# Performance work log

Hardware: AMD Instinct MI355X
Metric: run time of the kernel (lower is better)

Reference implementation:

```python
import jax, jax.numpy as jnp
import numpy as np

EPS = 1e-5
TEMPERATURE = 0.07

def _layernorm(x, g, b):
    m = jnp.mean(x, axis=-1, keepdims=True)
    v = jnp.mean(jnp.square(x - m), axis=-1, keepdims=True)
    return (x - m) * jax.lax.rsqrt(v + EPS) * g + b

def _proj(x, W, b, g, beta):
    # Linear -> LayerNorm -> ReLU (Dropout is identity in eval)
    return jax.nn.relu(_layernorm(x @ W + b, g, beta))

def setup_inputs() -> dict:
    key = jax.random.key(0)
    B, S, Dv, Dl, D = 8, 2048, 768, 768, 768
    ks = jax.random.split(key, 8)
    def lin(k, din, dout):
        return jax.random.normal(k, (din, dout), jnp.float32) / np.sqrt(din)
    return {
        "vision_features": jax.random.normal(ks[0], (B, S, Dv), jnp.float32),
        "language_features": jax.random.normal(ks[1], (B, S, Dl), jnp.float32),
        "vW": lin(ks[2], Dv, D), "vb": jnp.zeros((D,), jnp.float32),
        "vg": jnp.ones((D,), jnp.float32), "vbeta": jnp.zeros((D,), jnp.float32),
        "lW": lin(ks[3], Dl, D), "lb": jnp.zeros((D,), jnp.float32),
        "lg": jnp.ones((D,), jnp.float32), "lbeta": jnp.zeros((D,), jnp.float32),
        "claw": lin(ks[4], D, D),  # claw_matrix parameter [D, D]
        "oW": lin(ks[5], 2 * D, D), "ob": jnp.zeros((D,), jnp.float32),
        "og": jnp.ones((D,), jnp.float32), "obeta": jnp.zeros((D,), jnp.float32),
    }

def reference(vision_features, language_features, vW, vb, vg, vbeta,
              lW, lb, lg, lbeta, claw, oW, ob, og, obeta):
    vp = _proj(vision_features, vW, vb, vg, vbeta)      # [B,S,D]
    lp = _proj(language_features, lW, lb, lg, lbeta)    # [B,S,D]
    # similarity / temperature, scaled by mean of learned claw matrix
    sim = jnp.einsum('bsd,btd->bst', vp, lp) * (claw.mean() / TEMPERATURE)
    A = jax.nn.softmax(sim, axis=-1)                    # [B,S,S] claw matrix
    aligned_vision = jnp.einsum('bst,btd->bsd', A, vp)  # A @ vp
    aligned_language = jnp.einsum('bst,bsd->btd', A, lp)  # A^T @ lp
    combined = jnp.concatenate([aligned_vision, aligned_language], axis=-1)
    return jax.nn.relu(_layernorm(combined @ oW + ob, og, obeta))
```

## Files before the change

### kernel.cpp

```cpp
#include <hip/hip_runtime.h>
#include <hip/hip_bf16.h>

typedef short short8 __attribute__((ext_vector_type(8)));
typedef float f32x4 __attribute__((ext_vector_type(4)));
typedef unsigned short u16;

#define BK 32
static __device__ __forceinline__ int sw(int row, int g) {
  return row * 32 + ((g ^ ((row >> 3) & 3)) << 3);
}

static __device__ __forceinline__ u16 f2b(float f) {
  union { float f; unsigned u; } x; x.f = f;
  unsigned r = x.u + 0x7FFF + ((x.u >> 16) & 1);
  return (u16)(r >> 16);
}
static __device__ __forceinline__ float b2f(u16 u) {
  unsigned int x = ((unsigned int)u) << 16;
  float f; __builtin_memcpy(&f, &x, 4);
  return f;
}

static __device__ __forceinline__ void load8(const u16* p, u16* dst) {
  union { uint4 u; u16 h[8]; } t;
  t.u = *(const uint4*)p;
  #pragma unroll
  for (int j = 0; j < 8; ++j) dst[j] = t.h[j];
}
static __device__ __forceinline__ void load8(const float* p, u16* dst) {
  float4 a = ((const float4*)p)[0];
  float4 b = ((const float4*)p)[1];
  dst[0] = f2b(a.x); dst[1] = f2b(a.y); dst[2] = f2b(a.z); dst[3] = f2b(a.w);
  dst[4] = f2b(b.x); dst[5] = f2b(b.y); dst[6] = f2b(b.z); dst[7] = f2b(b.w);
}

static __device__ __forceinline__ void gl_lds16(const u16* g, u16* l) {
  __builtin_amdgcn_global_load_lds(
      (const __attribute__((address_space(1))) unsigned int*)g,
      (__attribute__((address_space(3))) unsigned int*)l, 16, 0, 0);
}

template<int MA, int MB, typename TyA, typename TyB, typename OutT>
__global__ __launch_bounds__(256) void gemm128(
    const TyA* __restrict__ A, const TyB* __restrict__ B,
    const float* __restrict__ bias, const float* __restrict__ alpha_ptr,
    OutT* __restrict__ C, int K, int lda, int ldb, int ldc,
    long long sA, long long sB, long long sC)
{
  __shared__ u16 As[128 * 32];
  __shared__ u16 Bs[128 * 32];

  A += (long long)blockIdx.z * sA;
  B += (long long)blockIdx.z * sB;
  C += (long long)blockIdx.z * sC;

  const int tid  = threadIdx.x;
  const int m0   = blockIdx.y * 128;
  const int n0   = blockIdx.x * 128;
  const int w    = tid >> 6, lane = tid & 63;
  const int wm   = (w >> 1) * 64;
  const int wn   = (w & 1) * 64;
  const int lrow = lane & 15;
  const int lg   = lane >> 4;

  int aoff[4], boff[4];
  #pragma unroll
  for (int t = 0; t < 4; ++t) {
    const int ar = wm + t * 16 + lrow;
    const int br = wn + t * 16 + lrow;
    aoff[t] = (MA == 1) ? sw(ar, lg) : ar * 32 + lg * 8;
    boff[t] = (MB == 1) ? sw(br, lg) : br * 32 + lg * 8;
  }

  f32x4 acc[4][4] = {};

  for (int k0 = 0; k0 < K; k0 += BK) {
    if constexpr (MA == 0) {
      gl_lds16(A + (long long)(m0 + (tid >> 2)) * lda + (k0 + (tid & 3) * 8),
               As + tid * 8);
      gl_lds16(A + (long long)(m0 + 64 + (tid >> 2)) * lda + (k0 + (tid & 3) * 8),
               As + 2048 + tid * 8);
    } else if constexpr (MA == 1) {
      const int kk = tid >> 3;
      #pragma unroll
      for (int p = 0; p < 2; ++p) {
        const int rr = (tid & 7) * 8 + p * 64;
        u16 h[8];
        load8(A + (long long)(k0 + kk) * lda + (m0 + rr), h);
        #pragma unroll
        for (int j = 0; j < 8; ++j) As[sw(rr + j, kk >> 3) + (kk & 7)] = h[j];
      }
    } else {
      const int g = tid & 3;
      #pragma unroll
      for (int p = 0; p < 2; ++p) {
        const int r = (tid >> 2) + p * 64;
        union { uint4 u; u16 h[8]; } t;
        load8(A + (long long)(m0 + r) * lda + (k0 + g * 8), t.h);
        *(uint4*)(As + r * 32 + g * 8) = t.u;
      }
    }
    if constexpr (MB == 0) {
      gl_lds16(B + (long long)(n0 + (tid >> 2)) * ldb + (k0 + (tid & 3) * 8),
               Bs + tid * 8);
      gl_lds16(B + (long long)(n0 + 64 + (tid >> 2)) * ldb + (k0 + (tid & 3) * 8),
               Bs + 2048 + tid * 8);
    } else {
      const int kk = tid >> 3;
      #pragma unroll
      for (int p = 0; p < 2; ++p) {
        const int rr = (tid & 7) * 8 + p * 64;
        u16 h[8];
        load8(B + (long long)(k0 + kk) * ldb + (n0 + rr), h);
        #pragma unroll
        for (int j = 0; j < 8; ++j) Bs[sw(rr + j, kk >> 3) + (kk & 7)] = h[j];
      }
    }
    __syncthreads();

    short8 af[4], bf[4];
    #pragma unroll
    for (int t = 0; t < 4; ++t) af[t] = *(const short8*)(As + aoff[t]);
    #pragma unroll
    for (int t = 0; t < 4; ++t) bf[t] = *(const short8*)(Bs + boff[t]);
    #pragma unroll
    for (int mt = 0; mt < 4; ++mt)
      #pragma unroll
      for (int nt = 0; nt < 4; ++nt)
        acc[mt][nt] = __builtin_amdgcn_mfma_f32_16x16x32_bf16(
            af[mt], bf[nt], acc[mt][nt], 0, 0, 0);
    __syncthreads();
  }

  const float alpha = alpha_ptr ? *alpha_ptr : 1.0f;
  #pragma unroll
  for (int nt = 0; nt < 4; ++nt) {
    const int n = n0 + wn + nt * 16 + lrow;
    const float bv = bias ? bias[n] : 0.0f;
    #pragma unroll
    for (int mt = 0; mt < 4; ++mt) {
      #pragma unroll
      for (int r = 0; r < 4; ++r) {
        const int m = m0 + wm + mt * 16 + lg * 4 + r;
        C[(long long)m * ldc + n] = OutT(acc[mt][nt][r] * alpha + bv);
      }
    }
  }
}

template<typename OutT>
__global__ __launch_bounds__(256) void ln_relu_kernel(
    const float* __restrict__ x, const float* __restrict__ g,
    const float* __restrict__ beta, OutT* __restrict__ out)
{
  __shared__ float sa[4], sb[4];
  const float* xr = x + (long long)blockIdx.x * 768;
  float v[3]; float s = 0.f, ss = 0.f;
  #pragma unroll
  for (int j = 0; j < 3; ++j) {
    v[j] = xr[threadIdx.x + j * 256];
    s += v[j]; ss += v[j] * v[j];
  }
  #pragma unroll
  for (int off = 32; off; off >>= 1) {
    s  += __shfl_down(s, off);
    ss += __shfl_down(ss, off);
  }
  const int w = threadIdx.x >> 6, lane = threadIdx.x & 63;
  if (!lane) { sa[w] = s; sb[w] = ss; }
  __syncthreads();
  s  = sa[0] + sa[1] + sa[2] + sa[3];
  ss = sb[0] + sb[1] + sb[2] + sb[3];
  const float mean = s * (1.f / 768.f);
  const float var  = ss * (1.f / 768.f) - mean * mean;
  const float rst  = rsqrtf(var + 1e-5f);
  OutT* orow = out + (long long)blockIdx.x * 768;
  #pragma unroll
  for (int j = 0; j < 3; ++j) {
    const int idx = threadIdx.x + j * 256;
    const float yv = (v[j] - mean) * rst * g[idx] + beta[idx];
    const float rv = (yv <= 0.f) ? 0.f : yv;
    orow[idx] = OutT(rv);
  }
}

__global__ __launch_bounds__(256) void softmax_kernel(u16* __restrict__ sim)
{
  __shared__ float sm[4], ssum[4];
  u16* row = sim + (long long)blockIdx.x * 2048;
  union { uint4 u; u16 h[8]; } v;
  v.u = *(const uint4*)(row + threadIdx.x * 8);
  float f[8]; float mx = -1e30f;
  #pragma unroll
  for (int j = 0; j < 8; ++j) { f[j] = b2f(v.h[j]); mx = fmaxf(mx, f[j]); }
  #pragma unroll
  for (int off = 32; off; off >>= 1) mx = fmaxf(mx, __shfl_down(mx, off));
  const int w = threadIdx.x >> 6, lane = threadIdx.x & 63;
  if (!lane) sm[w] = mx;
  __syncthreads();
  mx = fmaxf(fmaxf(sm[0], sm[1]), fmaxf(sm[2], sm[3]));
  float s = 0.f;
  #pragma unroll
  for (int j = 0; j < 8; ++j) { f[j] = __expf(f[j] - mx); s += f[j]; }
  #pragma unroll
  for (int off = 32; off; off >>= 1) s += __shfl_down(s, off);
  if (!lane) ssum[w] = s;
  __syncthreads();
  s = ssum[0] + ssum[1] + ssum[2] + ssum[3];
  const float inv = 1.f / s;
  #pragma unroll
  for (int j = 0; j < 8; ++j) v.h[j] = f2b(f[j] * inv);
  *(uint4*)(row + threadIdx.x * 8) = v.u;
}

__global__ __launch_bounds__(256) void claw_partial_kernel(
    const float* __restrict__ claw, float* __restrict__ partial, int n)
{
  __shared__ float sa[4];
  float s = 0.f;
  const int nv = n >> 2;
  for (int i = blockIdx.x * 256 + threadIdx.x; i < nv; i += 64 * 256) {
    float4 v = ((const float4*)claw)[i];
    s += v.x + v.y + v.z + v.w;
  }
  #pragma unroll
  for (int off = 32; off; off >>= 1) s += __shfl_down(s, off);
  const int w = threadIdx.x >> 6, lane = threadIdx.x & 63;
  if (!lane) sa[w] = s;
  __syncthreads();
  if (threadIdx.x == 0)
    partial[blockIdx.x] = sa[0] + sa[1] + sa[2] + sa[3];
}

__global__ void claw_final_kernel(
    const float* __restrict__ partial, float* __restrict__ scale, float inv)
{
  float s = partial[threadIdx.x];
  #pragma unroll
  for (int off = 32; off; off >>= 1) s += __shfl_down(s, off);
  if (threadIdx.x == 0) *scale = s * inv;
}

extern "C" void kernel_launch(void* const* d_in, const int* in_sizes, int n_in,
                              void* d_out, int out_size, void* d_ws, size_t ws_size,
                              hipStream_t stream)
{
  const float* vis   = (const float*)d_in[0];
  const float* lang  = (const float*)d_in[1];
  const float* vW    = (const float*)d_in[2];
  const float* vb    = (const float*)d_in[3];
  const float* vg    = (const float*)d_in[4];
  const float* vbeta = (const float*)d_in[5];
  const float* lW    = (const float*)d_in[6];
  const float* lb    = (const float*)d_in[7];
  const float* lg    = (const float*)d_in[8];
  const float* lbeta = (const float*)d_in[9];
  const float* claw  = (const float*)d_in[10];
  const float* oW    = (const float*)d_in[11];
  const float* ob    = (const float*)d_in[12];
  const float* og    = (const float*)d_in[13];
  const float* obeta = (const float*)d_in[14];
  float* out = (float*)d_out;

  constexpr int NB = 8, S = 2048, D = 768;
  constexpr int R = NB * S;
  constexpr long long SD = (long long)S * D;
  constexpr long long SS = (long long)S * S;
  const int nclaw = in_sizes[10];
  const float claw_inv = 1.0f / ((float)nclaw * 0.07f);
  const dim3 blk(256);

  char* ws = (char*)d_ws;
  u16*   vp      = (u16*)  (ws);
  u16*   lp      = (u16*)  (ws + 25165824);
  u16*   comb    = (u16*)  (ws + 50331648);
  u16*   sim     = (u16*)  (ws + 100663296);
  float* y       = (float*)(ws + 100663296);
  float* scale   = (float*)(ws + 167772160);
  float* partial = (float*)(ws + 167772176);

  claw_partial_kernel<<<64, blk, 0, stream>>>(claw, partial, nclaw);
  claw_final_kernel<<<1, 64, 0, stream>>>(partial, scale, claw_inv);

  gemm128<2, 1, float, float, float>
      <<<dim3(D / 128, R / 128, 1), blk, 0, stream>>>(
      vis, vW, vb, nullptr, y, D, D, D, D, 0, 0, 0);
  ln_relu_kernel<__hip_bfloat16><<<R, blk, 0, stream>>>(
      y, vg, vbeta, (__hip_bfloat16*)vp);

  gemm128<2, 1, float, float, float>
      <<<dim3(D / 128, R / 128, 1), blk, 0, stream>>>(
      lang, lW, lb, nullptr, y, D, D, D, D, 0, 0, 0);
  ln_relu_kernel<__hip_bfloat16><<<R, blk, 0, stream>>>(
      y, lg, lbeta, (__hip_bfloat16*)lp);

  gemm128<0, 0, u16, u16, __hip_bfloat16>
      <<<dim3(S / 128, S / 128, NB), blk, 0, stream>>>(
      vp, lp, nullptr, scale, (__hip_bfloat16*)sim, D, D, D, S, SD, SD, SS);
  softmax_kernel<<<R, blk, 0, stream>>>(sim);

  gemm128<0, 1, u16, u16, __hip_bfloat16>
      <<<dim3(D / 128, S / 128, NB), blk, 0, stream>>>(
      sim, vp, nullptr, nullptr, (__hip_bfloat16*)comb,
      S, S, D, 2 * D, SS, SD, 2 * SD);
  gemm128<1, 1, u16, u16, __hip_bfloat16>
      <<<dim3(D / 128, S / 128, NB), blk, 0, stream>>>(
      sim, lp, nullptr, nullptr, (__hip_bfloat16*)comb + D,
      S, S, D, 2 * D, SS, SD, 2 * SD);

  gemm128<0, 1, u16, float, float>
      <<<dim3(D / 128, R / 128, 1), blk, 0, stream>>>(
      comb, oW, ob, nullptr, y, 2 * D, 2 * D, D, D, 0, 0, 0);
  ln_relu_kernel<float><<<R, blk, 0, stream>>>(y, og, obeta, out);
}
```

Before: 675.8 us.

## Pre-transpose B operands and pre-convert fp32 inputs to bf16 for async LDS loads

Adds transpose and fp32-to-bf16 conversion kernels so that every GEMM can use the direct global-to-LDS load path (MA=0/MB=0) for B, and for A in all but the A^T GEMM. Before this, the GEMMs used scalar strided loads with per-element LDS scatter. Weights, inputs, vp and lp are transposed or converted ahead of time. The workspace is reused aggressively, with comb aliasing vp and vpT aliasing visb. The cost is the extra transpose and convert passes over global memory.

```diff
diff --git a/kernel.cpp b/kernel.cpp
--- a/kernel.cpp
+++ b/kernel.cpp
@@ -40,9 +40,9 @@
       (__attribute__((address_space(3))) unsigned int*)l, 16, 0, 0);
 }
 
-template<int MA, int MB, typename TyA, typename TyB, typename OutT>
+template<int MA, int MB, typename OutT>
 __global__ __launch_bounds__(256) void gemm128(
-    const TyA* __restrict__ A, const TyB* __restrict__ B,
+    const u16* __restrict__ A, const u16* __restrict__ B,
     const float* __restrict__ bias, const float* __restrict__ alpha_ptr,
     OutT* __restrict__ C, int K, int lda, int ldb, int ldc,
     long long sA, long long sB, long long sC)
@@ -80,7 +80,7 @@
                As + tid * 8);
       gl_lds16(A + (long long)(m0 + 64 + (tid >> 2)) * lda + (k0 + (tid & 3) * 8),
                As + 2048 + tid * 8);
-    } else if constexpr (MA == 1) {
+    } else {
       const int kk = tid >> 3;
       #pragma unroll
       for (int p = 0; p < 2; ++p) {
@@ -89,15 +89,6 @@
         load8(A + (long long)(k0 + kk) * lda + (m0 + rr), h);
         #pragma unroll
         for (int j = 0; j < 8; ++j) As[sw(rr + j, kk >> 3) + (kk & 7)] = h[j];
-      }
-    } else {
-      const int g = tid & 3;
-      #pragma unroll
-      for (int p = 0; p < 2; ++p) {
-        const int r = (tid >> 2) + p * 64;
-        union { uint4 u; u16 h[8]; } t;
-        load8(A + (long long)(m0 + r) * lda + (k0 + g * 8), t.h);
-        *(uint4*)(As + r * 32 + g * 8) = t.u;
       }
     }
     if constexpr (MB == 0) {
@@ -148,6 +139,49 @@
   }
 }
 
+template<typename T>
+__global__ __launch_bounds__(256) void transpose_kernel(
+    const T* __restrict__ in, u16* __restrict__ out, int R, int C,
+    long long sIn, long long sOut)
+{
+  __shared__ u16 t[64][66];
+  in  += (long long)blockIdx.z * sIn;
+  out += (long long)blockIdx.z * sOut;
+  const int r0 = blockIdx.y * 64, c0 = blockIdx.x * 64;
+  const int tid = threadIdx.x;
+  const int rr = tid >> 3, cc = (tid & 7) * 8;
+  #pragma unroll
+  for (int p = 0; p < 2; ++p) {
+    union { uint4 u; unsigned w[4]; u16 h[8]; } v;
+    const int row = rr + p * 32;
+    load8(in + (long long)(r0 + row) * C + (c0 + cc), v.h);
+    #pragma unroll
+    for (int k = 0; k < 4; ++k)
+      *(unsigned*)&t[row][cc + k * 2] = v.w[k];
+  }
+  __syncthreads();
+  #pragma unroll
+  for (int p = 0; p < 2; ++p) {
+    const int oc = (tid >> 3) + p * 32;
+    const int rc = (tid & 7) * 8;
+    union { uint4 u; u16 h[8]; } g;
+    #pragma unroll
+    for (int j = 0; j < 8; ++j) g.h[j] = t[rc + j][oc];
+    *(uint4*)(out + (long long)(c0 + oc) * R + (r0 + rc)) = g.u;
+  }
+}
+
+__global__ __launch_bounds__(256) void cvt_kernel(
+    const float* __restrict__ in, u16* __restrict__ out, int n8)
+{
+  const int stride = gridDim.x * 256;
+  for (int i = blockIdx.x * 256 + threadIdx.x; i < n8; i += stride) {
+    union { uint4 u; u16 h[8]; } v;
+    load8(in + (long long)i * 8, v.h);
+    *(uint4*)(out + (long long)i * 8) = v.u;
+  }
+}
+
 template<typename OutT>
 __global__ __launch_bounds__(256) void ln_relu_kernel(
     const float* __restrict__ x, const float* __restrict__ g,
@@ -271,45 +305,60 @@
   const dim3 blk(256);
 
   char* ws = (char*)d_ws;
-  u16*   vp      = (u16*)  (ws);
-  u16*   lp      = (u16*)  (ws + 25165824);
-  u16*   comb    = (u16*)  (ws + 50331648);
-  u16*   sim     = (u16*)  (ws + 100663296);
-  float* y       = (float*)(ws + 100663296);
+  u16*   vp    = (u16*)  (ws);
+  u16*   lp    = (u16*)  (ws + 25165824);
+  u16*   visb  = (u16*)  (ws + 50331648);
+  u16*   vpT   = (u16*)  (ws + 50331648);
+  u16*   langb = (u16*)  (ws + 75497472);
+  u16*   lpT   = (u16*)  (ws + 75497472);
+  u16*   sim   = (u16*)  (ws + 100663296);
+  float* y     = (float*)(ws + 100663296);
+  u16*   vWT   = (u16*)  (ws + 150994944);
+  u16*   lWT   = vWT + 589824;
+  u16*   oWT   = (u16*)  (ws + 150994944);
+  u16*   comb  = (u16*)  (ws);
   float* scale   = (float*)(ws + 167772160);
   float* partial = (float*)(ws + 167772176);
 
   claw_partial_kernel<<<64, blk, 0, stream>>>(claw, partial, nclaw);
   claw_final_kernel<<<1, 64, 0, stream>>>(partial, scale, claw_inv);
 
-  gemm128<2, 1, float, float, float>
-      <<<dim3(D / 128, R / 128, 1), blk, 0, stream>>>(
-      vis, vW, vb, nullptr, y, D, D, D, D, 0, 0, 0);
+  transpose_kernel<float><<<dim3(12, 12, 1), blk, 0, stream>>>(
+      vW, vWT, D, D, 0, 0);
+  transpose_kernel<float><<<dim3(12, 12, 1), blk, 0, stream>>>(
+      lW, lWT, D, D, 0, 0);
+
+  cvt_kernel<<<2048, blk, 0, stream>>>(vis, visb, (int)(R * D / 8));
+  gemm128<0, 0, float><<<dim3(D / 128, R / 128, 1), blk, 0, stream>>>(
+      visb, vWT, vb, nullptr, y, D, D, D, D, 0, 0, 0);
   ln_relu_kernel<__hip_bfloat16><<<R, blk, 0, stream>>>(
       y, vg, vbeta, (__hip_bfloat16*)vp);
-
-  gemm128<2, 1, float, float, float>
-      <<<dim3(D / 128, R / 128, 1), blk, 0, stream>>>(
-      lang, lW, lb, nullptr, y, D, D, D, D, 0, 0, 0);
+  transpose_kernel<u16><<<dim3(D / 64, S / 64, NB), blk, 0, stream>>>(
+      vp, vpT, S, D, SD, SD);
+
+  cvt_kernel<<<2048, blk, 0, stream>>>(lang, langb, (int)(R * D / 8));
+  gemm128<0, 0, float><<<dim3(D / 128, R / 128, 1), blk, 0, stream>>>(
+      langb, lWT, lb, nullptr, y, D, D, D, D, 0, 0, 0);
   ln_relu_kernel<__hip_bfloat16><<<R, blk, 0, stream>>>(
       y, lg, lbeta, (__hip_bfloat16*)lp);
-
-  gemm128<0, 0, u16, u16, __hip_bfloat16>
-      <<<dim3(S / 128, S / 128, NB), blk, 0, stream>>>(
+  transpose_kernel<u16><<<dim3(D / 64, S / 64, NB), blk, 0, stream>>>(
+      lp, lpT, S, D, SD, SD);
+
+  gemm128<0, 0, __hip_bfloat16><<<dim3(S / 128, S / 128, NB), blk, 0, stream>>>(
       vp, lp, nullptr, scale, (__hip_bfloat16*)sim, D, D, D, S, SD, SD, SS);
   softmax_kernel<<<R, blk, 0, stream>>>(sim);
 
-  gemm128<0, 1, u16, u16, __hip_bfloat16>
-      <<<dim3(D / 128, S / 128, NB), blk, 0, stream>>>(
-      sim, vp, nullptr, nullptr, (__hip_bfloat16*)comb,
-      S, S, D, 2 * D, SS, SD, 2 * SD);
-  gemm128<1, 1, u16, u16, __hip_bfloat16>
-      <<<dim3(D / 128, S / 128, NB), blk, 0, stream>>>(
-      sim, lp, nullptr, nullptr, (__hip_bfloat16*)comb + D,
-      S, S, D, 2 * D, SS, SD, 2 * SD);
-
-  gemm128<0, 1, u16, float, float>
-      <<<dim3(D / 128, R / 128, 1), blk, 0, stream>>>(
-      comb, oW, ob, nullptr, y, 2 * D, 2 * D, D, D, 0, 0, 0);
+  gemm128<0, 0, __hip_bfloat16><<<dim3(D / 128, S / 128, NB), blk, 0, stream>>>(
+      sim, vpT, nullptr, nullptr, (__hip_bfloat16*)comb,
+      S, S, S, 2 * D, SS, SD, 2 * SD);
+  gemm128<1, 0, __hip_bfloat16><<<dim3(D / 128, S / 128, NB), blk, 0, stream>>>(
+      sim, lpT, nullptr, nullptr, (__hip_bfloat16*)comb + D,
+      S, S, S, 2 * D, SS, SD, 2 * SD);
+
+  transpose_kernel<float><<<dim3(12, 24, 1), blk, 0, stream>>>(
+      oW, oWT, 2 * D, D, 0, 0);
+
+  gemm128<0, 0, float><<<dim3(D / 128, R / 128, 1), blk, 0, stream>>>(
+      comb, oWT, ob, nullptr, y, 2 * D, 2 * D, 2 * D, D, 0, 0, 0);
   ln_relu_kernel<float><<<R, blk, 0, stream>>>(y, og, obeta, out);
 }
```

New measurement: 645.4 us. 1.05x faster.
